# Kernel tuning notes

Hardware: AMD Instinct MI355X
Metric: run time of the kernel (lower is better)

## Reference

```python
import jax, jax.numpy as jnp
import numpy as np


def setup_inputs() -> dict:
    key = jax.random.key(0)
    k0, k1, k2, k3, k4, k5 = jax.random.split(key, 6)
    L1, L2, B, D = 512, 512, 32, 1024
    inputs1 = jax.random.normal(k0, (L1, B, D), dtype=jnp.float32)
    inputs2 = jax.random.normal(k1, (L2, B, D), dtype=jnp.float32)
    # mask value 0 marks a valid token (module keeps pairs where both masks == 0)
    mask1 = jax.random.randint(k2, (L1, B), 0, 2, dtype=jnp.int64)
    mask2 = jax.random.randint(k3, (L2, B), 0, 2, dtype=jnp.int64)
    W = jax.random.normal(k4, (D, D), dtype=jnp.float32) * 0.02
    b = jax.random.normal(k5, (1,), dtype=jnp.float32) * 0.02
    return {"inputs1": inputs1, "inputs2": inputs2, "mask1": mask1,
            "mask2": mask2, "W": W, "b": b, "k": 256}


def reference(inputs1, inputs2, mask1, mask2, W, b, k):
    # inputs: [len, bsz, hdim]; masks: [len, bsz]
    H1 = jnp.transpose(inputs1, (1, 0, 2))  # [B, L1, D]
    H2 = jnp.transpose(inputs2, (1, 0, 2))  # [B, L2, D]
    # bilinear scores: H1 @ W @ H2^T + b, then relu  -> [B, L1, L2]
    S = jax.nn.relu(jnp.einsum('bid,de,bje->bij', H1, W, H2) + b[0])
    # pair is valid iff both mask entries are 0
    valid = (mask1.T[:, :, None] == 0) & (mask2.T[:, None, :] == 0)  # [B, L1, L2]
    B = S.shape[0]
    S_flat = jnp.where(valid.reshape(B, -1), S.reshape(B, -1), -jnp.inf)
    num_elems = S_flat.shape[1]
    k_actual = min(k, num_elems)
    q, _ = jax.lax.top_k(S_flat, k_actual)  # [B, k_actual]
    # replace -inf tail entries with the last finite value in each row
    neg = jnp.isneginf(q)
    q_num_finite = k_actual - neg.sum(axis=-1)  # [B]
    fill = jnp.take_along_axis(q, (q_num_finite - 1)[:, None], axis=1)  # [B, 1]
    q = jnp.where(neg, fill, q)
    if k_actual < k:
        q = jnp.concatenate(
            [q, jnp.broadcast_to(q[:, -1:], (B, k - k_actual))], axis=1)
    return q
```

## Files before the change

kernel.cpp:

```cpp
#include <hip/hip_runtime.h>

typedef __bf16 bf16_t;
typedef bf16_t bf16x8 __attribute__((ext_vector_type(8)));
typedef float floatx4 __attribute__((ext_vector_type(4)));

#define L1C 512
#define L2C 512
#define BC  32
#define DC  1024
#define KTOP 256
#define NBIN 4096
#define CAP  512
#define NT   64
#define FBUF 16384

__device__ __forceinline__ unsigned short f2bf(float f) {
    unsigned u = __float_as_uint(f);
    u += 0x7FFFu + ((u >> 16) & 1u);
    return (unsigned short)(u >> 16);
}

__device__ __forceinline__ void g2l16(const unsigned short* g, unsigned short* l) {
    __builtin_amdgcn_global_load_lds((const unsigned int*)g, (unsigned int*)l,
                                     16, 0, 0);
}

__device__ __forceinline__ float decode_key(unsigned k) {
    return __uint_as_float(k & 0x7FFFFFFFu);
}

#define CFENCE asm volatile("" ::: "memory")

__global__ __launch_bounds__(512) void scan_kernel(
    const int* __restrict__ mask1, const int* __restrict__ mask2,
    int* __restrict__ idx1, int* __restrict__ idx2,
    unsigned* __restrict__ nv1, unsigned* __restrict__ nv2,
    unsigned* __restrict__ cnt) {
    __shared__ unsigned sc[512];
    int b = blockIdx.x, t = threadIdx.x;
    for (int which = 0; which < 2; which++) {
        const int* m = which ? mask2 : mask1;
        int* idx = which ? idx2 : idx1;
        unsigned v = (m[t * BC + b] == 0) ? 1u : 0u;
        sc[t] = v;
        __syncthreads();
        for (int off = 1; off < 512; off <<= 1) {
            unsigned x = (t >= off) ? sc[t - off] : 0u;
            __syncthreads();
            sc[t] += x;
            __syncthreads();
        }
        if (v) idx[b * 512 + sc[t] - 1] = t;
        if (t == 511) { if (which) nv2[b] = sc[511]; else nv1[b] = sc[511]; }
        __syncthreads();
    }
    if (t < NT) cnt[b * NT + t] = 0;
}

__global__ __launch_bounds__(256) void prep_kernel(
    const float* __restrict__ in1, const float* __restrict__ in2,
    const float* __restrict__ W,
    const int* __restrict__ idx1, const int* __restrict__ idx2,
    const unsigned* __restrict__ nv1, const unsigned* __restrict__ nv2,
    unsigned short* __restrict__ A1c, unsigned short* __restrict__ A2c,
    unsigned short* __restrict__ Wb) {
    int r = blockIdx.x, t = threadIdx.x;
    const float* src;
    unsigned short* dst;
    if (r < 2 * 16384) {
        int which = r >> 14;
        int rr = r & 16383;
        int b = rr >> 9, vi = rr & 511;
        unsigned nv = which ? nv2[b] : nv1[b];
        unsigned pad = (nv + 63u) & ~63u;
        if ((unsigned)vi >= pad) return;
        dst = (which ? A2c : A1c) + ((size_t)b * 512 + vi) * DC;
        if ((unsigned)vi < nv) {
            int l = (which ? idx2 : idx1)[b * 512 + vi];
            src = (which ? in2 : in1) + (size_t)(l * BC + b) * DC;
        } else {
            ushort4 z = {0, 0, 0, 0};
            reinterpret_cast<ushort4*>(dst)[t] = z;
            return;
        }
    } else {
        int r3 = r - 2 * 16384;
        src = W + (size_t)r3 * DC;
        dst = Wb + (size_t)r3 * DC;
    }
    float4 v = reinterpret_cast<const float4*>(src)[t];
    ushort4 o;
    o.x = f2bf(v.x); o.y = f2bf(v.y); o.z = f2bf(v.z); o.w = f2bf(v.w);
    reinterpret_cast<ushort4*>(dst)[t] = o;
}

__global__ __launch_bounds__(256) void gemm1_kernel(
    const unsigned short* __restrict__ A,
    const unsigned short* __restrict__ Bt,
    unsigned short* __restrict__ C,
    const unsigned* __restrict__ nv2) {
    int bi = blockIdx.x >> 2, mt = blockIdx.x & 3;
    unsigned pad2 = (nv2[bi] + 63u) & ~63u;
    if ((unsigned)(mt * 128) >= pad2) return;
    __shared__ unsigned short As0[2][128][32];
    __shared__ unsigned short Bs0[2][128][32];
    __shared__ unsigned short As1[2][128][32];
    __shared__ unsigned short Bs1[2][128][32];
    int tid = threadIdx.x;
    int wave = tid >> 6, lane = tid & 63;
    int lane15 = lane & 15, quad = lane >> 4;
    int wm = wave >> 1, wn = wave & 1;
    size_t m0 = (size_t)bi * 512 + mt * 128;
    size_t n0 = (size_t)blockIdx.y * 128;

    floatx4 zero = {0.f, 0.f, 0.f, 0.f};
    floatx4 acc[4][4];
#pragma unroll
    for (int i = 0; i < 4; i++)
#pragma unroll
        for (int j = 0; j < 4; j++) acc[i][j] = zero;

    auto stage = [&](unsigned short* la, unsigned short* lb, int k0) {
#pragma unroll
        for (int c = 0; c < 4; c++) {
            int cid = c * 256 + tid;
            int h = cid >> 9, row = (cid >> 2) & 127, col8 = (cid & 3) * 8;
            g2l16(&A[(m0 + row) * DC + k0 + h * 32 + col8],
                  la + (c * 256 + wave * 64) * 8);
        }
#pragma unroll
        for (int c = 0; c < 4; c++) {
            int cid = c * 256 + tid;
            int h = cid >> 9, row = (cid >> 2) & 127, col8 = (cid & 3) * 8;
            g2l16(&Bt[(n0 + row) * DC + k0 + h * 32 + col8],
                  lb + (c * 256 + wave * 64) * 8);
        }
    };

    stage(&As0[0][0][0], &Bs0[0][0][0], 0);
#pragma unroll
    for (int t = 0; t < DC / 64; t++) {
        const unsigned short* curA = (t & 1) ? &As1[0][0][0] : &As0[0][0][0];
        const unsigned short* curB = (t & 1) ? &Bs1[0][0][0] : &Bs0[0][0][0];
        if (t + 1 < DC / 64) {
            unsigned short* nxtA = (t & 1) ? &As0[0][0][0] : &As1[0][0][0];
            unsigned short* nxtB = (t & 1) ? &Bs0[0][0][0] : &Bs1[0][0][0];
            stage(nxtA, nxtB, (t + 1) * 64);
            asm volatile("s_waitcnt vmcnt(8)" ::: "memory");
        } else {
            asm volatile("s_waitcnt vmcnt(0)" ::: "memory");
        }
        __builtin_amdgcn_s_barrier();
        CFENCE;
#pragma unroll
        for (int h = 0; h < 2; h++) {
            bf16x8 af[4], bfr[4];
#pragma unroll
            for (int mi = 0; mi < 4; mi++)
                af[mi] = *reinterpret_cast<const bf16x8*>(
                    curA + h * 4096 + (wm * 64 + mi * 16 + lane15) * 32 + quad * 8);
#pragma unroll
            for (int ni = 0; ni < 4; ni++)
                bfr[ni] = *reinterpret_cast<const bf16x8*>(
                    curB + h * 4096 + (wn * 64 + ni * 16 + lane15) * 32 + quad * 8);
#pragma unroll
            for (int mi = 0; mi < 4; mi++)
#pragma unroll
                for (int ni = 0; ni < 4; ni++)
                    acc[mi][ni] = __builtin_amdgcn_mfma_f32_16x16x32_bf16(
                        af[mi], bfr[ni], acc[mi][ni], 0, 0, 0);
        }
        if (t + 1 < DC / 64) {
            CFENCE;
            __builtin_amdgcn_s_barrier();
            CFENCE;
        }
    }
#pragma unroll
    for (int mi = 0; mi < 4; mi++)
#pragma unroll
        for (int ni = 0; ni < 4; ni++)
#pragma unroll
            for (int r = 0; r < 4; r++) {
                size_t row = m0 + wm * 64 + mi * 16 + quad * 4 + r;
                size_t col = n0 + wn * 64 + ni * 16 + lane15;
                C[row * DC + col] = f2bf(acc[mi][ni][r]);
            }
}

__global__ __launch_bounds__(256) void gemm2_kernel(
    const unsigned short* __restrict__ A1c,
    const unsigned short* __restrict__ V,
    const unsigned* __restrict__ nv1, const unsigned* __restrict__ nv2,
    const float* __restrict__ bptr,
    unsigned* __restrict__ cand,
    unsigned* __restrict__ cnt) {
    int L = blockIdx.x;
    int xcd = L & 7, tile = (L >> 3) & 63, chunk = L >> 9;
    int b = xcd + (chunk << 3);
    int tx = tile & 7, ty = tile >> 3;
    int m0 = ty * 64, n0 = tx * 64;
    int gblk = b * NT + tile;
    int tid = threadIdx.x;
    unsigned nv1v = nv1[b], nv2v = nv2[b];
    unsigned pad1 = (nv1v + 63u) & ~63u, pad2 = (nv2v + 63u) & ~63u;
    if ((unsigned)m0 >= pad1 || (unsigned)n0 >= pad2) {
        if (tid == 0) cnt[gblk] = 0;
        return;
    }
    __shared__ unsigned short As0[2][64][32];
    __shared__ unsigned short Bs0[2][64][32];
    __shared__ unsigned short As1[2][64][32];
    __shared__ unsigned short Bs1[2][64][32];
    __shared__ unsigned lh[NBIN];
    __shared__ unsigned csum[256];
    __shared__ unsigned sel_c, sel_a, tsh, lcnt, zeq;
    int wave = tid >> 6, lane = tid & 63;
    int lane15 = lane & 15, quad = lane >> 4;
    const unsigned short* Ab = A1c + (size_t)b * 512 * DC;
    const unsigned short* Bb = V + (size_t)b * 512 * DC;

    for (int i = tid; i < NBIN; i += 256) lh[i] = 0;
    if (tid == 0) { sel_c = 0xFFFFFFFFu; lcnt = 0; zeq = 0; }

    floatx4 zero = {0.f, 0.f, 0.f, 0.f};
    floatx4 acc[4];
#pragma unroll
    for (int i = 0; i < 4; i++) acc[i] = zero;

    auto stage = [&](unsigned short* la, unsigned short* lb, int k0) {
#pragma unroll
        for (int c = 0; c < 2; c++) {
            int cid = c * 256 + tid;
            int h = cid >> 8, row = (cid >> 2) & 63, col8 = (cid & 3) * 8;
            g2l16(&Ab[(size_t)(m0 + row) * DC + k0 + h * 32 + col8],
                  la + (c * 256 + wave * 64) * 8);
            g2l16(&Bb[(size_t)(n0 + row) * DC + k0 + h * 32 + col8],
                  lb + (c * 256 + wave * 64) * 8);
        }
    };

    stage(&As0[0][0][0], &Bs0[0][0][0], 0);
#pragma unroll
    for (int t = 0; t < DC / 64; t++) {
        const unsigned short* curA = (t & 1) ? &As1[0][0][0] : &As0[0][0][0];
        const unsigned short* curB = (t & 1) ? &Bs1[0][0][0] : &Bs0[0][0][0];
        if (t + 1 < DC / 64) {
            unsigned short* nxtA = (t & 1) ? &As0[0][0][0] : &As1[0][0][0];
            unsigned short* nxtB = (t & 1) ? &Bs0[0][0][0] : &Bs1[0][0][0];
            stage(nxtA, nxtB, (t + 1) * 64);
            asm volatile("s_waitcnt vmcnt(4)" ::: "memory");
        } else {
            asm volatile("s_waitcnt vmcnt(0)" ::: "memory");
        }
        __builtin_amdgcn_s_barrier();
        CFENCE;
#pragma unroll
        for (int h = 0; h < 2; h++) {
            bf16x8 af, bfr[4];
            af = *reinterpret_cast<const bf16x8*>(
                curA + h * 2048 + (wave * 16 + lane15) * 32 + quad * 8);
#pragma unroll
            for (int ni = 0; ni < 4; ni++)
                bfr[ni] = *reinterpret_cast<const bf16x8*>(
                    curB + h * 2048 + (ni * 16 + lane15) * 32 + quad * 8);
#pragma unroll
            for (int ni = 0; ni < 4; ni++)
                acc[ni] = __builtin_amdgcn_mfma_f32_16x16x32_bf16(
                    af, bfr[ni], acc[ni], 0, 0, 0);
        }
        CFENCE;
        __builtin_amdgcn_s_barrier();
        CFENCE;
    }

    float bias = bptr[0];
    unsigned zc = 0;
#pragma unroll
    for (int ni = 0; ni < 4; ni++) {
        int jl = n0 + ni * 16 + lane15;
        int v2 = (unsigned)jl < nv2v;
#pragma unroll
        for (int r = 0; r < 4; r++) {
            int il = m0 + wave * 16 + quad * 4 + r;
            float s = acc[ni][r] + bias;
            if (v2 && (unsigned)il < nv1v) {
                if (s > 0.f)
                    atomicAdd(&lh[(__float_as_uint(s) | 0x80000000u) >> 20], 1u);
                else
                    zc++;
            }
        }
    }
    if (zc) atomicAdd(&lh[2048], zc);
    __syncthreads();
    unsigned s16 = 0;
#pragma unroll
    for (int i = 0; i < 16; i++) s16 += lh[tid * 16 + i];
    csum[tid] = s16;
    __syncthreads();
    for (int off = 1; off < 256; off <<= 1) {
        unsigned v = (tid + off < 256) ? csum[tid + off] : 0u;
        __syncthreads();
        csum[tid] += v;
        __syncthreads();
    }
    {
        unsigned above = (tid < 255) ? csum[tid + 1] : 0u;
        if (tid >= 128 && csum[tid] >= KTOP && above < KTOP) {
            sel_c = (unsigned)tid; sel_a = above;
        }
    }
    __syncthreads();
    if (tid == 0) {
        if (sel_c == 0xFFFFFFFFu) {
            tsh = 2048u << 20;
        } else {
            unsigned cum = sel_a, bin = 2048;
            for (int bb = (int)sel_c * 16 + 15; bb >= (int)sel_c * 16; --bb) {
                unsigned hb = lh[bb];
                if (cum + hb >= KTOP) { bin = (unsigned)bb; break; }
                cum += hb;
            }
            tsh = bin << 20;
        }
    }
    __syncthreads();
    unsigned T = tsh;
    unsigned base = (unsigned)gblk * CAP;
#pragma unroll
    for (int ni = 0; ni < 4; ni++) {
        int jl = n0 + ni * 16 + lane15;
        int v2 = (unsigned)jl < nv2v;
#pragma unroll
        for (int r = 0; r < 4; r++) {
            int il = m0 + wave * 16 + quad * 4 + r;
            float s = acc[ni][r] + bias;
            s = s > 0.f ? s : 0.f;
            unsigned key = (v2 && (unsigned)il < nv1v)
                               ? (__float_as_uint(s) | 0x80000000u) : 0u;
            if (key > T) {
                unsigned p = atomicAdd(&lcnt, 1u);
                if (p < CAP) cand[base + p] = key;
            } else if (key == T) {
                unsigned z = atomicAdd(&zeq, 1u);
                if (z < KTOP) {
                    unsigned p = atomicAdd(&lcnt, 1u);
                    if (p < CAP) cand[base + p] = key;
                }
            }
        }
    }
    __syncthreads();
    if (tid == 0) cnt[gblk] = lcnt < CAP ? lcnt : CAP;
}

__global__ __launch_bounds__(1024) void final_kernel(
    const unsigned* __restrict__ cand, const unsigned* __restrict__ cnt,
    float* __restrict__ out) {
    __shared__ unsigned buf[FBUF];
    __shared__ unsigned h[NBIN];
    __shared__ unsigned ss[256];
    __shared__ unsigned scnt_s[NT], off_s[NT];
    __shared__ unsigned ntot_s, sel_c, sel_a, B_s, R_s, mcount;
    __shared__ int have_s;
    __shared__ unsigned srt[256];
    int b = blockIdx.x, tid = threadIdx.x;
    int wv = tid >> 6, ln = tid & 63;

    if (tid < NT) {
        unsigned c = cnt[b * NT + tid];
        scnt_s[tid] = c < CAP ? c : CAP;
    }
    __syncthreads();
    if (tid == 0) {
        unsigned o = 0;
        for (int i = 0; i < NT; i++) {
            unsigned c = scnt_s[i];
            if (o + c > FBUF) c = (o < FBUF) ? FBUF - o : 0;
            scnt_s[i] = c;
            off_s[i] = o;
            o += c;
        }
        ntot_s = o;
        have_s = 1;
    }
    __syncthreads();
    for (int s = wv; s < NT; s += 16) {
        unsigned c = scnt_s[s], o = off_s[s];
        const unsigned* p = cand + (size_t)(b * NT + s) * CAP;
        for (unsigned i = ln; i < c; i += 64) buf[o + i] = p[i];
    }
    __syncthreads();
    unsigned n = ntot_s;

    unsigned Kr = KTOP;
    unsigned pfx = 0;
    unsigned kth = 0;
    for (int pass = 0; pass < 3; pass++) {
        int bins = (pass < 2) ? NBIN : 256;
        int shift = (pass == 0) ? 20 : (pass == 1) ? 8 : 0;
        int nch = bins >> 4;
        for (int i = tid; i < bins; i += 1024) h[i] = 0;
        __syncthreads();
        for (unsigned i = tid; i < n; i += 1024) {
            unsigned k = buf[i];
            bool ok = (pass == 0) ||
                      (pass == 1 && (k >> 20) == pfx) ||
                      (pass == 2 && (k >> 8) == pfx);
            if (ok) atomicAdd(&h[(k >> shift) & (bins - 1)], 1u);
        }
        __syncthreads();
        if (tid < nch) {
            unsigned s = 0;
#pragma unroll
            for (int i = 0; i < 16; i++) s += h[tid * 16 + i];
            ss[tid] = s;
        }
        __syncthreads();
        for (int off = 1; off < nch; off <<= 1) {
            unsigned v = 0;
            if (tid < nch && tid + (unsigned)off < (unsigned)nch) v = ss[tid + off];
            __syncthreads();
            if (tid < nch) ss[tid] += v;
            __syncthreads();
        }
        if (pass == 0) {
            if (tid == 0) have_s = (ss[0] >= KTOP);
            __syncthreads();
            if (!have_s) break;
        }
        if (tid < nch) {
            unsigned above = (tid + 1 < (unsigned)nch) ? ss[tid + 1] : 0u;
            if (above < Kr && ss[tid] >= Kr) { sel_c = tid; sel_a = above; }
        }
        __syncthreads();
        if (tid == 0) {
            unsigned cum = sel_a;
            for (int bb = (int)sel_c * 16 + 15; bb >= (int)sel_c * 16; --bb) {
                unsigned hb = h[bb];
                if (cum + hb >= Kr) { B_s = (unsigned)bb; R_s = Kr - cum; break; }
                cum += hb;
            }
        }
        __syncthreads();
        unsigned Bv = B_s;
        Kr = R_s;
        if (pass == 0) pfx = Bv;
        else if (pass == 1) pfx = (pfx << 12) | Bv;
        else kth = (pfx << 8) | Bv;
        __syncthreads();
    }

    if (tid == 0) mcount = 0;
    __syncthreads();
    int have = have_s;
    unsigned lim = have ? kth : 0u;
    for (unsigned i = tid; i < n; i += 1024) {
        unsigned k = buf[i];
        if (k > lim) {
            unsigned p = atomicAdd(&mcount, 1u);
            if (p < 256) srt[p] = k;
        }
    }
    __syncthreads();
    unsigned m = mcount;
    if (tid < 256 && tid >= (int)m) srt[tid] = have ? kth : 0u;
    for (int k2 = 2; k2 <= 256; k2 <<= 1) {
        for (int j2 = k2 >> 1; j2 > 0; j2 >>= 1) {
            __syncthreads();
            if (tid < 256) {
                int ixj = tid ^ j2;
                if (ixj > tid) {
                    unsigned a = srt[tid], c = srt[ixj];
                    bool up = (tid & k2) == 0;
                    if (up ? (a < c) : (a > c)) { srt[tid] = c; srt[ixj] = a; }
                }
            }
        }
    }
    __syncthreads();
    if (tid < 256) {
        unsigned nval = have ? KTOP : (m < KTOP ? m : KTOP);
        float v;
        if ((unsigned)tid < nval) v = decode_key(srt[tid]);
        else v = (nval > 0) ? decode_key(srt[nval - 1]) : -__builtin_inff();
        out[b * KTOP + tid] = v;
    }
}

extern "C" void kernel_launch(void* const* d_in, const int* in_sizes, int n_in,
                              void* d_out, int out_size, void* d_ws, size_t ws_size,
                              hipStream_t stream) {
    const float* in1   = (const float*)d_in[0];
    const float* in2   = (const float*)d_in[1];
    const int*   mask1 = (const int*)d_in[2];
    const int*   mask2 = (const int*)d_in[3];
    const float* W     = (const float*)d_in[4];
    const float* bias  = (const float*)d_in[5];
    float* out = (float*)d_out;

    char* ws = (char*)d_ws;
    size_t off = 0;
    const size_t nElem = (size_t)512 * BC * DC;
    unsigned short* A1c = (unsigned short*)(ws + off); off += nElem * 2;
    unsigned short* A2c = (unsigned short*)(ws + off); off += nElem * 2;
    unsigned short* Wb  = (unsigned short*)(ws + off); off += (size_t)DC * DC * 2;
    unsigned short* V   = (unsigned short*)(ws + off); off += nElem * 2;
    unsigned* cand = (unsigned*)(ws + off); off += (size_t)BC * NT * CAP * 4;
    unsigned* cnt  = (unsigned*)(ws + off); off += (size_t)BC * NT * 4;
    int* idx1 = (int*)(ws + off); off += (size_t)BC * 512 * 4;
    int* idx2 = (int*)(ws + off); off += (size_t)BC * 512 * 4;
    unsigned* nv1 = (unsigned*)(ws + off); off += BC * 4;
    unsigned* nv2 = (unsigned*)(ws + off); off += BC * 4;

    scan_kernel<<<BC, 512, 0, stream>>>(mask1, mask2, idx1, idx2, nv1, nv2, cnt);
    prep_kernel<<<2 * 16384 + 1024, 256, 0, stream>>>(
        in1, in2, W, idx1, idx2, nv1, nv2, A1c, A2c, Wb);
    gemm1_kernel<<<dim3(128, 8), 256, 0, stream>>>(A2c, Wb, V, nv2);
    gemm2_kernel<<<2048, 256, 0, stream>>>(A1c, V, nv1, nv2, bias, cand, cnt);
    final_kernel<<<BC, 1024, 0, stream>>>(cand, cnt, out);
}
```

Before: 246.0 us.

## Enlarge gemm2 tiles to 128x128 and use 8-wave blocks in gemm1

The per-batch score GEMM now uses 128x128 output tiles, 16 per batch, with each wave computing a 64x64 sub-tile. The histogram buffer is aliased onto the staging LDS once the K loop finishes, which keeps shared memory in bounds. Each loaded A/B fragment is reused across more MFMAs, and fewer candidate blocks feed the final merge (NT goes from 64 to 16). Separately, gemm1 runs 512 threads per block with a 2x4 wave grid, each wave holding a 64x32 accumulator. The trade-off is fewer gemm2 blocks (512), lower occupancy, coarser skipping of padded tiles, and more values per block histogram and candidate buffer, so CAP could overflow.

Result: slower. 251.7 us (+2.3%).

```diff
diff --git a/kernel.cpp b/kernel.cpp
--- a/kernel.cpp
+++ b/kernel.cpp
@@ -11,7 +11,7 @@
 #define KTOP 256
 #define NBIN 4096
 #define CAP  512
-#define NT   64
+#define NT   16
 #define FBUF 16384
 
 __device__ __forceinline__ unsigned short f2bf(float f) {
@@ -94,7 +94,7 @@
     reinterpret_cast<ushort4*>(dst)[t] = o;
 }
 
-__global__ __launch_bounds__(256) void gemm1_kernel(
+__global__ __launch_bounds__(512) void gemm1_kernel(
     const unsigned short* __restrict__ A,
     const unsigned short* __restrict__ Bt,
     unsigned short* __restrict__ C,
@@ -109,134 +109,31 @@
     int tid = threadIdx.x;
     int wave = tid >> 6, lane = tid & 63;
     int lane15 = lane & 15, quad = lane >> 4;
-    int wm = wave >> 1, wn = wave & 1;
+    int wm = wave >> 2, wn = wave & 3;
     size_t m0 = (size_t)bi * 512 + mt * 128;
     size_t n0 = (size_t)blockIdx.y * 128;
 
     floatx4 zero = {0.f, 0.f, 0.f, 0.f};
-    floatx4 acc[4][4];
+    floatx4 acc[4][2];
 #pragma unroll
     for (int i = 0; i < 4; i++)
 #pragma unroll
-        for (int j = 0; j < 4; j++) acc[i][j] = zero;
+        for (int j = 0; j < 2; j++) acc[i][j] = zero;
 
     auto stage = [&](unsigned short* la, unsigned short* lb, int k0) {
 #pragma unroll
-        for (int c = 0; c < 4; c++) {
-            int cid = c * 256 + tid;
+        for (int c = 0; c < 2; c++) {
+            int cid = c * 512 + tid;
             int h = cid >> 9, row = (cid >> 2) & 127, col8 = (cid & 3) * 8;
             g2l16(&A[(m0 + row) * DC + k0 + h * 32 + col8],
-                  la + (c * 256 + wave * 64) * 8);
-        }
-#pragma unroll
-        for (int c = 0; c < 4; c++) {
-            int cid = c * 256 + tid;
+                  la + (c * 512 + wave * 64) * 8);
+        }
+#pragma unroll
+        for (int c = 0; c < 2; c++) {
+            int cid = c * 512 + tid;
             int h = cid >> 9, row = (cid >> 2) & 127, col8 = (cid & 3) * 8;
             g2l16(&Bt[(n0 + row) * DC + k0 + h * 32 + col8],
-                  lb + (c * 256 + wave * 64) * 8);
-        }
-    };
-
-    stage(&As0[0][0][0], &Bs0[0][0][0], 0);
-#pragma unroll
-    for (int t = 0; t < DC / 64; t++) {
-        const unsigned short* curA = (t & 1) ? &As1[0][0][0] : &As0[0][0][0];
-        const unsigned short* curB = (t & 1) ? &Bs1[0][0][0] : &Bs0[0][0][0];
-        if (t + 1 < DC / 64) {
-            unsigned short* nxtA = (t & 1) ? &As0[0][0][0] : &As1[0][0][0];
-            unsigned short* nxtB = (t & 1) ? &Bs0[0][0][0] : &Bs1[0][0][0];
-            stage(nxtA, nxtB, (t + 1) * 64);
-            asm volatile("s_waitcnt vmcnt(8)" ::: "memory");
-        } else {
-            asm volatile("s_waitcnt vmcnt(0)" ::: "memory");
-        }
-        __builtin_amdgcn_s_barrier();
-        CFENCE;
-#pragma unroll
-        for (int h = 0; h < 2; h++) {
-            bf16x8 af[4], bfr[4];
-#pragma unroll
-            for (int mi = 0; mi < 4; mi++)
-                af[mi] = *reinterpret_cast<const bf16x8*>(
-                    curA + h * 4096 + (wm * 64 + mi * 16 + lane15) * 32 + quad * 8);
-#pragma unroll
-            for (int ni = 0; ni < 4; ni++)
-                bfr[ni] = *reinterpret_cast<const bf16x8*>(
-                    curB + h * 4096 + (wn * 64 + ni * 16 + lane15) * 32 + quad * 8);
-#pragma unroll
-            for (int mi = 0; mi < 4; mi++)
-#pragma unroll
-                for (int ni = 0; ni < 4; ni++)
-                    acc[mi][ni] = __builtin_amdgcn_mfma_f32_16x16x32_bf16(
-                        af[mi], bfr[ni], acc[mi][ni], 0, 0, 0);
-        }
-        if (t + 1 < DC / 64) {
-            CFENCE;
-            __builtin_amdgcn_s_barrier();
-            CFENCE;
-        }
-    }
-#pragma unroll
-    for (int mi = 0; mi < 4; mi++)
-#pragma unroll
-        for (int ni = 0; ni < 4; ni++)
-#pragma unroll
-            for (int r = 0; r < 4; r++) {
-                size_t row = m0 + wm * 64 + mi * 16 + quad * 4 + r;
-                size_t col = n0 + wn * 64 + ni * 16 + lane15;
-                C[row * DC + col] = f2bf(acc[mi][ni][r]);
-            }
-}
-
-__global__ __launch_bounds__(256) void gemm2_kernel(
-    const unsigned short* __restrict__ A1c,
-    const unsigned short* __restrict__ V,
-    const unsigned* __restrict__ nv1, const unsigned* __restrict__ nv2,
-    const float* __restrict__ bptr,
-    unsigned* __restrict__ cand,
-    unsigned* __restrict__ cnt) {
-    int L = blockIdx.x;
-    int xcd = L & 7, tile = (L >> 3) & 63, chunk = L >> 9;
-    int b = xcd + (chunk << 3);
-    int tx = tile & 7, ty = tile >> 3;
-    int m0 = ty * 64, n0 = tx * 64;
-    int gblk = b * NT + tile;
-    int tid = threadIdx.x;
-    unsigned nv1v = nv1[b], nv2v = nv2[b];
-    unsigned pad1 = (nv1v + 63u) & ~63u, pad2 = (nv2v + 63u) & ~63u;
-    if ((unsigned)m0 >= pad1 || (unsigned)n0 >= pad2) {
-        if (tid == 0) cnt[gblk] = 0;
-        return;
-    }
-    __shared__ unsigned short As0[2][64][32];
-    __shared__ unsigned short Bs0[2][64][32];
-    __shared__ unsigned short As1[2][64][32];
-    __shared__ unsigned short Bs1[2][64][32];
-    __shared__ unsigned lh[NBIN];
-    __shared__ unsigned csum[256];
-    __shared__ unsigned sel_c, sel_a, tsh, lcnt, zeq;
-    int wave = tid >> 6, lane = tid & 63;
-    int lane15 = lane & 15, quad = lane >> 4;
-    const unsigned short* Ab = A1c + (size_t)b * 512 * DC;
-    const unsigned short* Bb = V + (size_t)b * 512 * DC;
-
-    for (int i = tid; i < NBIN; i += 256) lh[i] = 0;
-    if (tid == 0) { sel_c = 0xFFFFFFFFu; lcnt = 0; zeq = 0; }
-
-    floatx4 zero = {0.f, 0.f, 0.f, 0.f};
-    floatx4 acc[4];
-#pragma unroll
-    for (int i = 0; i < 4; i++) acc[i] = zero;
-
-    auto stage = [&](unsigned short* la, unsigned short* lb, int k0) {
-#pragma unroll
-        for (int c = 0; c < 2; c++) {
-            int cid = c * 256 + tid;
-            int h = cid >> 8, row = (cid >> 2) & 63, col8 = (cid & 3) * 8;
-            g2l16(&Ab[(size_t)(m0 + row) * DC + k0 + h * 32 + col8],
-                  la + (c * 256 + wave * 64) * 8);
-            g2l16(&Bb[(size_t)(n0 + row) * DC + k0 + h * 32 + col8],
-                  lb + (c * 256 + wave * 64) * 8);
+                  lb + (c * 512 + wave * 64) * 8);
         }
     };
 
@@ -257,41 +154,161 @@
         CFENCE;
 #pragma unroll
         for (int h = 0; h < 2; h++) {
-            bf16x8 af, bfr[4];
-            af = *reinterpret_cast<const bf16x8*>(
-                curA + h * 2048 + (wave * 16 + lane15) * 32 + quad * 8);
+            bf16x8 af[4], bfr[2];
+#pragma unroll
+            for (int mi = 0; mi < 4; mi++)
+                af[mi] = *reinterpret_cast<const bf16x8*>(
+                    curA + h * 4096 + (wm * 64 + mi * 16 + lane15) * 32 + quad * 8);
+#pragma unroll
+            for (int ni = 0; ni < 2; ni++)
+                bfr[ni] = *reinterpret_cast<const bf16x8*>(
+                    curB + h * 4096 + (wn * 32 + ni * 16 + lane15) * 32 + quad * 8);
+#pragma unroll
+            for (int mi = 0; mi < 4; mi++)
+#pragma unroll
+                for (int ni = 0; ni < 2; ni++)
+                    acc[mi][ni] = __builtin_amdgcn_mfma_f32_16x16x32_bf16(
+                        af[mi], bfr[ni], acc[mi][ni], 0, 0, 0);
+        }
+        if (t + 1 < DC / 64) {
+            CFENCE;
+            __builtin_amdgcn_s_barrier();
+            CFENCE;
+        }
+    }
+#pragma unroll
+    for (int mi = 0; mi < 4; mi++)
+#pragma unroll
+        for (int ni = 0; ni < 2; ni++)
+#pragma unroll
+            for (int r = 0; r < 4; r++) {
+                size_t row = m0 + wm * 64 + mi * 16 + quad * 4 + r;
+                size_t col = n0 + wn * 32 + ni * 16 + lane15;
+                C[row * DC + col] = f2bf(acc[mi][ni][r]);
+            }
+}
+
+__global__ __launch_bounds__(256) void gemm2_kernel(
+    const unsigned short* __restrict__ A1c,
+    const unsigned short* __restrict__ V,
+    const unsigned* __restrict__ nv1, const unsigned* __restrict__ nv2,
+    const float* __restrict__ bptr,
+    unsigned* __restrict__ cand,
+    unsigned* __restrict__ cnt) {
+    int L = blockIdx.x;
+    int xcd = L & 7, idx = L >> 3;
+    int tile = idx & 15, chunk = idx >> 4;
+    int b = (chunk << 3) + xcd;
+    int tx = tile & 3, ty = tile >> 2;
+    int m0 = ty * 128, n0 = tx * 128;
+    int gblk = b * NT + tile;
+    int tid = threadIdx.x;
+    unsigned nv1v = nv1[b], nv2v = nv2[b];
+    unsigned pad1 = (nv1v + 63u) & ~63u, pad2 = (nv2v + 63u) & ~63u;
+    if ((unsigned)m0 >= pad1 || (unsigned)n0 >= pad2) {
+        if (tid == 0) cnt[gblk] = 0;
+        return;
+    }
+    __shared__ unsigned smem_u[16384];
+    unsigned short* As0 = (unsigned short*)smem_u;
+    unsigned short* Bs0 = As0 + 8192;
+    unsigned short* As1 = As0 + 16384;
+    unsigned short* Bs1 = As0 + 24576;
+    unsigned* lh = smem_u;
+    __shared__ unsigned csum[256];
+    __shared__ unsigned sel_c, sel_a, tsh, lcnt, zeq;
+    int wave = tid >> 6, lane = tid & 63;
+    int lane15 = lane & 15, quad = lane >> 4;
+    int wm = wave >> 1, wn = wave & 1;
+    const unsigned short* Ab = A1c + (size_t)b * 512 * DC;
+    const unsigned short* Bb = V + (size_t)b * 512 * DC;
+
+    floatx4 zero = {0.f, 0.f, 0.f, 0.f};
+    floatx4 acc[4][4];
+#pragma unroll
+    for (int i = 0; i < 4; i++)
+#pragma unroll
+        for (int j = 0; j < 4; j++) acc[i][j] = zero;
+
+    auto stage = [&](unsigned short* la, unsigned short* lb, int k0) {
+#pragma unroll
+        for (int c = 0; c < 4; c++) {
+            int cid = c * 256 + tid;
+            int h = cid >> 9, row = (cid >> 2) & 127, col8 = (cid & 3) * 8;
+            g2l16(&Ab[(size_t)(m0 + row) * DC + k0 + h * 32 + col8],
+                  la + (c * 256 + wave * 64) * 8);
+        }
+#pragma unroll
+        for (int c = 0; c < 4; c++) {
+            int cid = c * 256 + tid;
+            int h = cid >> 9, row = (cid >> 2) & 127, col8 = (cid & 3) * 8;
+            g2l16(&Bb[(size_t)(n0 + row) * DC + k0 + h * 32 + col8],
+                  lb + (c * 256 + wave * 64) * 8);
+        }
+    };
+
+    stage(As0, Bs0, 0);
+#pragma unroll
+    for (int t = 0; t < DC / 64; t++) {
+        const unsigned short* curA = (t & 1) ? As1 : As0;
+        const unsigned short* curB = (t & 1) ? Bs1 : Bs0;
+        if (t + 1 < DC / 64) {
+            unsigned short* nxtA = (t & 1) ? As0 : As1;
+            unsigned short* nxtB = (t & 1) ? Bs0 : Bs1;
+            stage(nxtA, nxtB, (t + 1) * 64);
+            asm volatile("s_waitcnt vmcnt(8)" ::: "memory");
+        } else {
+            asm volatile("s_waitcnt vmcnt(0)" ::: "memory");
+        }
+        __builtin_amdgcn_s_barrier();
+        CFENCE;
+#pragma unroll
+        for (int h = 0; h < 2; h++) {
+            bf16x8 af[4], bfr[4];
+#pragma unroll
+            for (int mi = 0; mi < 4; mi++)
+                af[mi] = *reinterpret_cast<const bf16x8*>(
+                    curA + h * 4096 + (wm * 64 + mi * 16 + lane15) * 32 + quad * 8);
 #pragma unroll
             for (int ni = 0; ni < 4; ni++)
                 bfr[ni] = *reinterpret_cast<const bf16x8*>(
-                    curB + h * 2048 + (ni * 16 + lane15) * 32 + quad * 8);
-#pragma unroll
-            for (int ni = 0; ni < 4; ni++)
-                acc[ni] = __builtin_amdgcn_mfma_f32_16x16x32_bf16(
-                    af, bfr[ni], acc[ni], 0, 0, 0);
+                    curB + h * 4096 + (wn * 64 + ni * 16 + lane15) * 32 + quad * 8);
+#pragma unroll
+            for (int mi = 0; mi < 4; mi++)
+#pragma unroll
+                for (int ni = 0; ni < 4; ni++)
+                    acc[mi][ni] = __builtin_amdgcn_mfma_f32_16x16x32_bf16(
+                        af[mi], bfr[ni], acc[mi][ni], 0, 0, 0);
         }
         CFENCE;
         __builtin_amdgcn_s_barrier();
         CFENCE;
     }
 
+    for (int i = tid; i < NBIN; i += 256) lh[i] = 0;
+    if (tid == 0) { sel_c = 0xFFFFFFFFu; lcnt = 0; zeq = 0; }
+    __syncthreads();
+
     float bias = bptr[0];
     unsigned zc = 0;
 #pragma unroll
-    for (int ni = 0; ni < 4; ni++) {
-        int jl = n0 + ni * 16 + lane15;
-        int v2 = (unsigned)jl < nv2v;
-#pragma unroll
-        for (int r = 0; r < 4; r++) {
-            int il = m0 + wave * 16 + quad * 4 + r;
-            float s = acc[ni][r] + bias;
-            if (v2 && (unsigned)il < nv1v) {
-                if (s > 0.f)
-                    atomicAdd(&lh[(__float_as_uint(s) | 0x80000000u) >> 20], 1u);
-                else
-                    zc++;
+    for (int mi = 0; mi < 4; mi++)
+#pragma unroll
+        for (int ni = 0; ni < 4; ni++) {
+            int jl = n0 + wn * 64 + ni * 16 + lane15;
+            int v2 = (unsigned)jl < nv2v;
+#pragma unroll
+            for (int r = 0; r < 4; r++) {
+                int il = m0 + wm * 64 + mi * 16 + quad * 4 + r;
+                float s = acc[mi][ni][r] + bias;
+                if (v2 && (unsigned)il < nv1v) {
+                    if (s > 0.f)
+                        atomicAdd(&lh[(__float_as_uint(s) | 0x80000000u) >> 20], 1u);
+                    else
+                        zc++;
+                }
             }
         }
-    }
     if (zc) atomicAdd(&lh[2048], zc);
     __syncthreads();
     unsigned s16 = 0;
@@ -329,28 +346,30 @@
     unsigned T = tsh;
     unsigned base = (unsigned)gblk * CAP;
 #pragma unroll
-    for (int ni = 0; ni < 4; ni++) {
-        int jl = n0 + ni * 16 + lane15;
-        int v2 = (unsigned)jl < nv2v;
-#pragma unroll
-        for (int r = 0; r < 4; r++) {
-            int il = m0 + wave * 16 + quad * 4 + r;
-            float s = acc[ni][r] + bias;
-            s = s > 0.f ? s : 0.f;
-            unsigned key = (v2 && (unsigned)il < nv1v)
-                               ? (__float_as_uint(s) | 0x80000000u) : 0u;
-            if (key > T) {
-                unsigned p = atomicAdd(&lcnt, 1u);
-                if (p < CAP) cand[base + p] = key;
-            } else if (key == T) {
-                unsigned z = atomicAdd(&zeq, 1u);
-                if (z < KTOP) {
+    for (int mi = 0; mi < 4; mi++)
+#pragma unroll
+        for (int ni = 0; ni < 4; ni++) {
+            int jl = n0 + wn * 64 + ni * 16 + lane15;
+            int v2 = (unsigned)jl < nv2v;
+#pragma unroll
+            for (int r = 0; r < 4; r++) {
+                int il = m0 + wm * 64 + mi * 16 + quad * 4 + r;
+                float s = acc[mi][ni][r] + bias;
+                s = s > 0.f ? s : 0.f;
+                unsigned key = (v2 && (unsigned)il < nv1v)
+                                   ? (__float_as_uint(s) | 0x80000000u) : 0u;
+                if (key > T) {
                     unsigned p = atomicAdd(&lcnt, 1u);
                     if (p < CAP) cand[base + p] = key;
+                } else if (key == T) {
+                    unsigned z = atomicAdd(&zeq, 1u);
+                    if (z < KTOP) {
+                        unsigned p = atomicAdd(&lcnt, 1u);
+                        if (p < CAP) cand[base + p] = key;
+                    }
                 }
             }
         }
-    }
     __syncthreads();
     if (tid == 0) cnt[gblk] = lcnt < CAP ? lcnt : CAP;
 }
@@ -517,7 +536,7 @@
     scan_kernel<<<BC, 512, 0, stream>>>(mask1, mask2, idx1, idx2, nv1, nv2, cnt);
     prep_kernel<<<2 * 16384 + 1024, 256, 0, stream>>>(
         in1, in2, W, idx1, idx2, nv1, nv2, A1c, A2c, Wb);
-    gemm1_kernel<<<dim3(128, 8), 256, 0, stream>>>(A2c, Wb, V, nv2);
-    gemm2_kernel<<<2048, 256, 0, stream>>>(A1c, V, nv1, nv2, bias, cand, cnt);
+    gemm1_kernel<<<dim3(128, 8), 512, 0, stream>>>(A2c, Wb, V, nv2);
+    gemm2_kernel<<<512, 256, 0, stream>>>(A1c, V, nv1, nv2, bias, cand, cnt);
     final_kernel<<<BC, 1024, 0, stream>>>(cand, cnt, out);
 }
```

## Compact gemm2 tiles into a persistent worklist and widen gemm1 to eight waves

Applied to the files above, without the earlier changes.

A new single-block kernel builds a compact list of the non-empty (batch, tile) pairs from the valid-token counts. gemm2 then runs as a persistent grid of 768 blocks that loops over only those tiles, instead of launching 2048 blocks where many exit early. gemm1 moves to 512 threads per block with a 2x4 wave layout, so each wave holds fewer accumulators and the block has more waves to hide latency. The cost is one extra kernel launch and extra per-tile barrier and histogram resets inside the persistent loop.

After: 244.0 us. Within noise of the previous version (-0.8%).

```diff
diff --git a/kernel.cpp b/kernel.cpp
--- a/kernel.cpp
+++ b/kernel.cpp
@@ -55,6 +55,30 @@
         __syncthreads();
     }
     if (t < NT) cnt[b * NT + t] = 0;
+}
+
+__global__ __launch_bounds__(256) void wl_kernel(
+    const unsigned* __restrict__ nv1, const unsigned* __restrict__ nv2,
+    unsigned* __restrict__ wl, unsigned* __restrict__ wcount) {
+    __shared__ unsigned t1s[BC], t2s[BC], offs[BC + 1];
+    int tid = threadIdx.x;
+    if (tid < BC) {
+        unsigned p1 = (nv1[tid] + 63u) & ~63u, p2 = (nv2[tid] + 63u) & ~63u;
+        t1s[tid] = p1 >> 6; t2s[tid] = p2 >> 6;
+    }
+    __syncthreads();
+    if (tid == 0) {
+        unsigned o = 0;
+        for (int b = 0; b < BC; b++) { offs[b] = o; o += t1s[b] * t2s[b]; }
+        offs[BC] = o;
+        *wcount = o;
+    }
+    __syncthreads();
+    for (int b = 0; b < BC; b++) {
+        unsigned nt = t1s[b] * t2s[b], o = offs[b], t2 = t2s[b];
+        for (unsigned i = tid; i < nt; i += 256)
+            wl[o + i] = ((unsigned)b << 6) | ((i / t2) << 3) | (i % t2);
+    }
 }
 
 __global__ __launch_bounds__(256) void prep_kernel(
@@ -94,7 +118,7 @@
     reinterpret_cast<ushort4*>(dst)[t] = o;
 }
 
-__global__ __launch_bounds__(256) void gemm1_kernel(
+__global__ __launch_bounds__(512) void gemm1_kernel(
     const unsigned short* __restrict__ A,
     const unsigned short* __restrict__ Bt,
     unsigned short* __restrict__ C,
@@ -109,134 +133,31 @@
     int tid = threadIdx.x;
     int wave = tid >> 6, lane = tid & 63;
     int lane15 = lane & 15, quad = lane >> 4;
-    int wm = wave >> 1, wn = wave & 1;
+    int wm = wave >> 2, wn = wave & 3;
     size_t m0 = (size_t)bi * 512 + mt * 128;
     size_t n0 = (size_t)blockIdx.y * 128;
 
     floatx4 zero = {0.f, 0.f, 0.f, 0.f};
-    floatx4 acc[4][4];
+    floatx4 acc[4][2];
 #pragma unroll
     for (int i = 0; i < 4; i++)
 #pragma unroll
-        for (int j = 0; j < 4; j++) acc[i][j] = zero;
+        for (int j = 0; j < 2; j++) acc[i][j] = zero;
 
     auto stage = [&](unsigned short* la, unsigned short* lb, int k0) {
 #pragma unroll
-        for (int c = 0; c < 4; c++) {
-            int cid = c * 256 + tid;
+        for (int c = 0; c < 2; c++) {
+            int cid = c * 512 + tid;
             int h = cid >> 9, row = (cid >> 2) & 127, col8 = (cid & 3) * 8;
             g2l16(&A[(m0 + row) * DC + k0 + h * 32 + col8],
-                  la + (c * 256 + wave * 64) * 8);
-        }
-#pragma unroll
-        for (int c = 0; c < 4; c++) {
-            int cid = c * 256 + tid;
+                  la + (c * 512 + wave * 64) * 8);
+        }
+#pragma unroll
+        for (int c = 0; c < 2; c++) {
+            int cid = c * 512 + tid;
             int h = cid >> 9, row = (cid >> 2) & 127, col8 = (cid & 3) * 8;
             g2l16(&Bt[(n0 + row) * DC + k0 + h * 32 + col8],
-                  lb + (c * 256 + wave * 64) * 8);
-        }
-    };
-
-    stage(&As0[0][0][0], &Bs0[0][0][0], 0);
-#pragma unroll
-    for (int t = 0; t < DC / 64; t++) {
-        const unsigned short* curA = (t & 1) ? &As1[0][0][0] : &As0[0][0][0];
-        const unsigned short* curB = (t & 1) ? &Bs1[0][0][0] : &Bs0[0][0][0];
-        if (t + 1 < DC / 64) {
-            unsigned short* nxtA = (t & 1) ? &As0[0][0][0] : &As1[0][0][0];
-            unsigned short* nxtB = (t & 1) ? &Bs0[0][0][0] : &Bs1[0][0][0];
-            stage(nxtA, nxtB, (t + 1) * 64);
-            asm volatile("s_waitcnt vmcnt(8)" ::: "memory");
-        } else {
-            asm volatile("s_waitcnt vmcnt(0)" ::: "memory");
-        }
-        __builtin_amdgcn_s_barrier();
-        CFENCE;
-#pragma unroll
-        for (int h = 0; h < 2; h++) {
-            bf16x8 af[4], bfr[4];
-#pragma unroll
-            for (int mi = 0; mi < 4; mi++)
-                af[mi] = *reinterpret_cast<const bf16x8*>(
-                    curA + h * 4096 + (wm * 64 + mi * 16 + lane15) * 32 + quad * 8);
-#pragma unroll
-            for (int ni = 0; ni < 4; ni++)
-                bfr[ni] = *reinterpret_cast<const bf16x8*>(
-                    curB + h * 4096 + (wn * 64 + ni * 16 + lane15) * 32 + quad * 8);
-#pragma unroll
-            for (int mi = 0; mi < 4; mi++)
-#pragma unroll
-                for (int ni = 0; ni < 4; ni++)
-                    acc[mi][ni] = __builtin_amdgcn_mfma_f32_16x16x32_bf16(
-                        af[mi], bfr[ni], acc[mi][ni], 0, 0, 0);
-        }
-        if (t + 1 < DC / 64) {
-            CFENCE;
-            __builtin_amdgcn_s_barrier();
-            CFENCE;
-        }
-    }
-#pragma unroll
-    for (int mi = 0; mi < 4; mi++)
-#pragma unroll
-        for (int ni = 0; ni < 4; ni++)
-#pragma unroll
-            for (int r = 0; r < 4; r++) {
-                size_t row = m0 + wm * 64 + mi * 16 + quad * 4 + r;
-                size_t col = n0 + wn * 64 + ni * 16 + lane15;
-                C[row * DC + col] = f2bf(acc[mi][ni][r]);
-            }
-}
-
-__global__ __launch_bounds__(256) void gemm2_kernel(
-    const unsigned short* __restrict__ A1c,
-    const unsigned short* __restrict__ V,
-    const unsigned* __restrict__ nv1, const unsigned* __restrict__ nv2,
-    const float* __restrict__ bptr,
-    unsigned* __restrict__ cand,
-    unsigned* __restrict__ cnt) {
-    int L = blockIdx.x;
-    int xcd = L & 7, tile = (L >> 3) & 63, chunk = L >> 9;
-    int b = xcd + (chunk << 3);
-    int tx = tile & 7, ty = tile >> 3;
-    int m0 = ty * 64, n0 = tx * 64;
-    int gblk = b * NT + tile;
-    int tid = threadIdx.x;
-    unsigned nv1v = nv1[b], nv2v = nv2[b];
-    unsigned pad1 = (nv1v + 63u) & ~63u, pad2 = (nv2v + 63u) & ~63u;
-    if ((unsigned)m0 >= pad1 || (unsigned)n0 >= pad2) {
-        if (tid == 0) cnt[gblk] = 0;
-        return;
-    }
-    __shared__ unsigned short As0[2][64][32];
-    __shared__ unsigned short Bs0[2][64][32];
-    __shared__ unsigned short As1[2][64][32];
-    __shared__ unsigned short Bs1[2][64][32];
-    __shared__ unsigned lh[NBIN];
-    __shared__ unsigned csum[256];
-    __shared__ unsigned sel_c, sel_a, tsh, lcnt, zeq;
-    int wave = tid >> 6, lane = tid & 63;
-    int lane15 = lane & 15, quad = lane >> 4;
-    const unsigned short* Ab = A1c + (size_t)b * 512 * DC;
-    const unsigned short* Bb = V + (size_t)b * 512 * DC;
-
-    for (int i = tid; i < NBIN; i += 256) lh[i] = 0;
-    if (tid == 0) { sel_c = 0xFFFFFFFFu; lcnt = 0; zeq = 0; }
-
-    floatx4 zero = {0.f, 0.f, 0.f, 0.f};
-    floatx4 acc[4];
-#pragma unroll
-    for (int i = 0; i < 4; i++) acc[i] = zero;
-
-    auto stage = [&](unsigned short* la, unsigned short* lb, int k0) {
-#pragma unroll
-        for (int c = 0; c < 2; c++) {
-            int cid = c * 256 + tid;
-            int h = cid >> 8, row = (cid >> 2) & 63, col8 = (cid & 3) * 8;
-            g2l16(&Ab[(size_t)(m0 + row) * DC + k0 + h * 32 + col8],
-                  la + (c * 256 + wave * 64) * 8);
-            g2l16(&Bb[(size_t)(n0 + row) * DC + k0 + h * 32 + col8],
-                  lb + (c * 256 + wave * 64) * 8);
+                  lb + (c * 512 + wave * 64) * 8);
         }
     };
 
@@ -257,102 +178,206 @@
         CFENCE;
 #pragma unroll
         for (int h = 0; h < 2; h++) {
-            bf16x8 af, bfr[4];
-            af = *reinterpret_cast<const bf16x8*>(
-                curA + h * 2048 + (wave * 16 + lane15) * 32 + quad * 8);
-#pragma unroll
-            for (int ni = 0; ni < 4; ni++)
+            bf16x8 af[4], bfr[2];
+#pragma unroll
+            for (int mi = 0; mi < 4; mi++)
+                af[mi] = *reinterpret_cast<const bf16x8*>(
+                    curA + h * 4096 + (wm * 64 + mi * 16 + lane15) * 32 + quad * 8);
+#pragma unroll
+            for (int ni = 0; ni < 2; ni++)
                 bfr[ni] = *reinterpret_cast<const bf16x8*>(
-                    curB + h * 2048 + (ni * 16 + lane15) * 32 + quad * 8);
-#pragma unroll
-            for (int ni = 0; ni < 4; ni++)
-                acc[ni] = __builtin_amdgcn_mfma_f32_16x16x32_bf16(
-                    af, bfr[ni], acc[ni], 0, 0, 0);
-        }
-        CFENCE;
-        __builtin_amdgcn_s_barrier();
-        CFENCE;
-    }
-
+                    curB + h * 4096 + (wn * 32 + ni * 16 + lane15) * 32 + quad * 8);
+#pragma unroll
+            for (int mi = 0; mi < 4; mi++)
+#pragma unroll
+                for (int ni = 0; ni < 2; ni++)
+                    acc[mi][ni] = __builtin_amdgcn_mfma_f32_16x16x32_bf16(
+                        af[mi], bfr[ni], acc[mi][ni], 0, 0, 0);
+        }
+        if (t + 1 < DC / 64) {
+            CFENCE;
+            __builtin_amdgcn_s_barrier();
+            CFENCE;
+        }
+    }
+#pragma unroll
+    for (int mi = 0; mi < 4; mi++)
+#pragma unroll
+        for (int ni = 0; ni < 2; ni++)
+#pragma unroll
+            for (int r = 0; r < 4; r++) {
+                size_t row = m0 + wm * 64 + mi * 16 + quad * 4 + r;
+                size_t col = n0 + wn * 32 + ni * 16 + lane15;
+                C[row * DC + col] = f2bf(acc[mi][ni][r]);
+            }
+}
+
+__global__ __launch_bounds__(256) void gemm2_kernel(
+    const unsigned short* __restrict__ A1c,
+    const unsigned short* __restrict__ V,
+    const unsigned* __restrict__ nv1, const unsigned* __restrict__ nv2,
+    const float* __restrict__ bptr,
+    unsigned* __restrict__ cand,
+    unsigned* __restrict__ cnt,
+    const unsigned* __restrict__ wl, const unsigned* __restrict__ wcount) {
+    __shared__ unsigned short As0[2][64][32];
+    __shared__ unsigned short Bs0[2][64][32];
+    __shared__ unsigned short As1[2][64][32];
+    __shared__ unsigned short Bs1[2][64][32];
+    __shared__ unsigned lh[NBIN];
+    __shared__ unsigned csum[256];
+    __shared__ unsigned sel_c, sel_a, tsh, lcnt, zeq;
+    int tid = threadIdx.x;
+    int wave = tid >> 6, lane = tid & 63;
+    int lane15 = lane & 15, quad = lane >> 4;
+    unsigned nwork = *wcount;
     float bias = bptr[0];
-    unsigned zc = 0;
-#pragma unroll
-    for (int ni = 0; ni < 4; ni++) {
-        int jl = n0 + ni * 16 + lane15;
-        int v2 = (unsigned)jl < nv2v;
-#pragma unroll
-        for (int r = 0; r < 4; r++) {
-            int il = m0 + wave * 16 + quad * 4 + r;
-            float s = acc[ni][r] + bias;
-            if (v2 && (unsigned)il < nv1v) {
-                if (s > 0.f)
-                    atomicAdd(&lh[(__float_as_uint(s) | 0x80000000u) >> 20], 1u);
-                else
-                    zc++;
-            }
-        }
-    }
-    if (zc) atomicAdd(&lh[2048], zc);
-    __syncthreads();
-    unsigned s16 = 0;
-#pragma unroll
-    for (int i = 0; i < 16; i++) s16 += lh[tid * 16 + i];
-    csum[tid] = s16;
-    __syncthreads();
-    for (int off = 1; off < 256; off <<= 1) {
-        unsigned v = (tid + off < 256) ? csum[tid + off] : 0u;
-        __syncthreads();
-        csum[tid] += v;
-        __syncthreads();
-    }
-    {
-        unsigned above = (tid < 255) ? csum[tid + 1] : 0u;
-        if (tid >= 128 && csum[tid] >= KTOP && above < KTOP) {
-            sel_c = (unsigned)tid; sel_a = above;
-        }
-    }
-    __syncthreads();
-    if (tid == 0) {
-        if (sel_c == 0xFFFFFFFFu) {
-            tsh = 2048u << 20;
-        } else {
-            unsigned cum = sel_a, bin = 2048;
-            for (int bb = (int)sel_c * 16 + 15; bb >= (int)sel_c * 16; --bb) {
-                unsigned hb = lh[bb];
-                if (cum + hb >= KTOP) { bin = (unsigned)bb; break; }
-                cum += hb;
-            }
-            tsh = bin << 20;
-        }
-    }
-    __syncthreads();
-    unsigned T = tsh;
-    unsigned base = (unsigned)gblk * CAP;
-#pragma unroll
-    for (int ni = 0; ni < 4; ni++) {
-        int jl = n0 + ni * 16 + lane15;
-        int v2 = (unsigned)jl < nv2v;
-#pragma unroll
-        for (int r = 0; r < 4; r++) {
-            int il = m0 + wave * 16 + quad * 4 + r;
-            float s = acc[ni][r] + bias;
-            s = s > 0.f ? s : 0.f;
-            unsigned key = (v2 && (unsigned)il < nv1v)
-                               ? (__float_as_uint(s) | 0x80000000u) : 0u;
-            if (key > T) {
-                unsigned p = atomicAdd(&lcnt, 1u);
-                if (p < CAP) cand[base + p] = key;
-            } else if (key == T) {
-                unsigned z = atomicAdd(&zeq, 1u);
-                if (z < KTOP) {
+    unsigned chunk = gridDim.x >> 3;
+    unsigned w0 = (blockIdx.x & 7) * chunk + (blockIdx.x >> 3);
+
+    for (unsigned w = w0; w < nwork; w += gridDim.x) {
+        unsigned d = wl[w];
+        int b = d >> 6, ty = (d >> 3) & 7, tx = d & 7;
+        int m0 = ty * 64, n0 = tx * 64;
+        int gblk = b * NT + ty * 8 + tx;
+        unsigned nv1v = nv1[b], nv2v = nv2[b];
+        const unsigned short* Ab = A1c + (size_t)b * 512 * DC;
+        const unsigned short* Bb = V + (size_t)b * 512 * DC;
+
+        for (int i = tid; i < NBIN; i += 256) lh[i] = 0;
+        if (tid == 0) { sel_c = 0xFFFFFFFFu; lcnt = 0; zeq = 0; }
+
+        floatx4 zero = {0.f, 0.f, 0.f, 0.f};
+        floatx4 acc[4];
+#pragma unroll
+        for (int i = 0; i < 4; i++) acc[i] = zero;
+
+        auto stage = [&](unsigned short* la, unsigned short* lb, int k0) {
+#pragma unroll
+            for (int c = 0; c < 2; c++) {
+                int cid = c * 256 + tid;
+                int h = cid >> 8, row = (cid >> 2) & 63, col8 = (cid & 3) * 8;
+                g2l16(&Ab[(size_t)(m0 + row) * DC + k0 + h * 32 + col8],
+                      la + (c * 256 + wave * 64) * 8);
+                g2l16(&Bb[(size_t)(n0 + row) * DC + k0 + h * 32 + col8],
+                      lb + (c * 256 + wave * 64) * 8);
+            }
+        };
+
+        stage(&As0[0][0][0], &Bs0[0][0][0], 0);
+#pragma unroll
+        for (int t = 0; t < DC / 64; t++) {
+            const unsigned short* curA = (t & 1) ? &As1[0][0][0] : &As0[0][0][0];
+            const unsigned short* curB = (t & 1) ? &Bs1[0][0][0] : &Bs0[0][0][0];
+            if (t + 1 < DC / 64) {
+                unsigned short* nxtA = (t & 1) ? &As0[0][0][0] : &As1[0][0][0];
+                unsigned short* nxtB = (t & 1) ? &Bs0[0][0][0] : &Bs1[0][0][0];
+                stage(nxtA, nxtB, (t + 1) * 64);
+                asm volatile("s_waitcnt vmcnt(4)" ::: "memory");
+            } else {
+                asm volatile("s_waitcnt vmcnt(0)" ::: "memory");
+            }
+            __builtin_amdgcn_s_barrier();
+            CFENCE;
+#pragma unroll
+            for (int h = 0; h < 2; h++) {
+                bf16x8 af, bfr[4];
+                af = *reinterpret_cast<const bf16x8*>(
+                    curA + h * 2048 + (wave * 16 + lane15) * 32 + quad * 8);
+#pragma unroll
+                for (int ni = 0; ni < 4; ni++)
+                    bfr[ni] = *reinterpret_cast<const bf16x8*>(
+                        curB + h * 2048 + (ni * 16 + lane15) * 32 + quad * 8);
+#pragma unroll
+                for (int ni = 0; ni < 4; ni++)
+                    acc[ni] = __builtin_amdgcn_mfma_f32_16x16x32_bf16(
+                        af, bfr[ni], acc[ni], 0, 0, 0);
+            }
+            CFENCE;
+            __builtin_amdgcn_s_barrier();
+            CFENCE;
+        }
+
+        unsigned zc = 0;
+#pragma unroll
+        for (int ni = 0; ni < 4; ni++) {
+            int jl = n0 + ni * 16 + lane15;
+            int v2 = (unsigned)jl < nv2v;
+#pragma unroll
+            for (int r = 0; r < 4; r++) {
+                int il = m0 + wave * 16 + quad * 4 + r;
+                float s = acc[ni][r] + bias;
+                if (v2 && (unsigned)il < nv1v) {
+                    if (s > 0.f)
+                        atomicAdd(&lh[(__float_as_uint(s) | 0x80000000u) >> 20], 1u);
+                    else
+                        zc++;
+                }
+            }
+        }
+        if (zc) atomicAdd(&lh[2048], zc);
+        __syncthreads();
+        unsigned s16 = 0;
+#pragma unroll
+        for (int i = 0; i < 16; i++) s16 += lh[tid * 16 + i];
+        csum[tid] = s16;
+        __syncthreads();
+        for (int off = 1; off < 256; off <<= 1) {
+            unsigned v = (tid + off < 256) ? csum[tid + off] : 0u;
+            __syncthreads();
+            csum[tid] += v;
+            __syncthreads();
+        }
+        {
+            unsigned above = (tid < 255) ? csum[tid + 1] : 0u;
+            if (tid >= 128 && csum[tid] >= KTOP && above < KTOP) {
+                sel_c = (unsigned)tid; sel_a = above;
+            }
+        }
+        __syncthreads();
+        if (tid == 0) {
+            if (sel_c == 0xFFFFFFFFu) {
+                tsh = 2048u << 20;
+            } else {
+                unsigned cum = sel_a, bin = 2048;
+                for (int bb = (int)sel_c * 16 + 15; bb >= (int)sel_c * 16; --bb) {
+                    unsigned hb = lh[bb];
+                    if (cum + hb >= KTOP) { bin = (unsigned)bb; break; }
+                    cum += hb;
+                }
+                tsh = bin << 20;
+            }
+        }
+        __syncthreads();
+        unsigned T = tsh;
+        unsigned base = (unsigned)gblk * CAP;
+#pragma unroll
+        for (int ni = 0; ni < 4; ni++) {
+            int jl = n0 + ni * 16 + lane15;
+            int v2 = (unsigned)jl < nv2v;
+#pragma unroll
+            for (int r = 0; r < 4; r++) {
+                int il = m0 + wave * 16 + quad * 4 + r;
+                float s = acc[ni][r] + bias;
+                s = s > 0.f ? s : 0.f;
+                unsigned key = (v2 && (unsigned)il < nv1v)
+                                   ? (__float_as_uint(s) | 0x80000000u) : 0u;
+                if (key > T) {
                     unsigned p = atomicAdd(&lcnt, 1u);
                     if (p < CAP) cand[base + p] = key;
+                } else if (key == T) {
+                    unsigned z = atomicAdd(&zeq, 1u);
+                    if (z < KTOP) {
+                        unsigned p = atomicAdd(&lcnt, 1u);
+                        if (p < CAP) cand[base + p] = key;
+                    }
                 }
             }
         }
-    }
-    __syncthreads();
-    if (tid == 0) cnt[gblk] = lcnt < CAP ? lcnt : CAP;
+        __syncthreads();
+        if (tid == 0) cnt[gblk] = lcnt < CAP ? lcnt : CAP;
+        __syncthreads();
+    }
 }
 
 __global__ __launch_bounds__(1024) void final_kernel(
@@ -513,11 +538,15 @@
     int* idx2 = (int*)(ws + off); off += (size_t)BC * 512 * 4;
     unsigned* nv1 = (unsigned*)(ws + off); off += BC * 4;
     unsigned* nv2 = (unsigned*)(ws + off); off += BC * 4;
+    unsigned* wl  = (unsigned*)(ws + off); off += 2048 * 4;
+    unsigned* wcount = (unsigned*)(ws + off); off += 4;
 
     scan_kernel<<<BC, 512, 0, stream>>>(mask1, mask2, idx1, idx2, nv1, nv2, cnt);
+    wl_kernel<<<1, 256, 0, stream>>>(nv1, nv2, wl, wcount);
     prep_kernel<<<2 * 16384 + 1024, 256, 0, stream>>>(
         in1, in2, W, idx1, idx2, nv1, nv2, A1c, A2c, Wb);
-    gemm1_kernel<<<dim3(128, 8), 256, 0, stream>>>(A2c, Wb, V, nv2);
-    gemm2_kernel<<<2048, 256, 0, stream>>>(A1c, V, nv1, nv2, bias, cand, cnt);
+    gemm1_kernel<<<dim3(128, 8), 512, 0, stream>>>(A2c, Wb, V, nv2);
+    gemm2_kernel<<<768, 256, 0, stream>>>(A1c, V, nv1, nv2, bias, cand, cnt,
+                                          wl, wcount);
     final_kernel<<<BC, 1024, 0, stream>>>(cand, cnt, out);
 }
```
